# Optimization experiments

Hardware: AMD Instinct MI355X
Metric: run time of the kernel (lower is better)

The kernel has to match this reference:

```python
import jax, jax.numpy as jnp
import numpy as np

DIM = 2048
H = 16
KVH = 4
HD = DIM // H          # 128
G = H // KVH           # 4
EPS = 1e-6


def _rmsnorm(x, w):
    rms = jnp.sqrt(jnp.mean(x * x, axis=-1, keepdims=True) + EPS)
    return x / rms * w


def setup_inputs() -> dict:
    key = jax.random.key(0)
    ks = jax.random.split(key, 9)
    B, S = 4, 2048
    query = jax.random.normal(ks[0], (B, S, DIM), dtype=jnp.float32)
    key_t = jax.random.normal(ks[1], (B, S, DIM), dtype=jnp.float32)
    value = jax.random.normal(ks[2], (B, S, DIM), dtype=jnp.float32)
    sc = 1.0 / np.sqrt(DIM)
    Wq = jax.random.normal(ks[3], (DIM, DIM), dtype=jnp.float32) * sc
    Wk = jax.random.normal(ks[4], (KVH * HD, DIM), dtype=jnp.float32) * sc
    Wv = jax.random.normal(ks[5], (KVH * HD, DIM), dtype=jnp.float32) * sc
    Wo = jax.random.normal(ks[6], (DIM, DIM), dtype=jnp.float32) * sc
    norm_q_w = jnp.ones((HD,), dtype=jnp.float32)
    norm_k_w = jnp.ones((HD,), dtype=jnp.float32)
    return {"query": query, "key": key_t, "value": value,
            "Wq": Wq, "Wk": Wk, "Wv": Wv, "Wo": Wo,
            "norm_q_w": norm_q_w, "norm_k_w": norm_k_w}


def reference(query, key, value, Wq, Wk, Wv, Wo, norm_q_w, norm_k_w):
    B, S, _ = query.shape
    Skv = key.shape[1]
    scale = HD ** -0.5
    # projections (torch Linear: x @ W.T)
    q = (query @ Wq.T).reshape(B, S, H, HD)
    k = (key @ Wk.T).reshape(B, Skv, KVH, HD)
    v = (value @ Wv.T).reshape(B, Skv, KVH, HD)
    # fused QK RMSNorm over head_dim
    q = _rmsnorm(q, norm_q_w)
    k = _rmsnorm(k, norm_k_w)
    # GQA: group query heads as (KVH, G); repeat_interleave maps q head
    # h = kv*G + g to kv head kv, which this reshape reproduces exactly.
    q = q.transpose(0, 2, 1, 3).reshape(B, KVH, G, S, HD)
    k = k.transpose(0, 2, 1, 3)  # [B, KVH, Skv, HD]
    v = v.transpose(0, 2, 1, 3)
    scores = jnp.einsum('bkgsd,bktd->bkgst', q, k) * scale
    attn = jax.nn.softmax(scores, axis=-1)
    out = jnp.einsum('bkgst,bktd->bkgsd', attn, v)
    # back to [B, S, H*HD] with head order (kv, g)
    out = out.transpose(0, 3, 1, 2, 4).reshape(B, S, DIM)
    return out @ Wo.T
```

## Files before the change

### kernel.cpp

```cpp
#include <hip/hip_runtime.h>
#include <hip/hip_bf16.h>


typedef short short8 __attribute__((ext_vector_type(8)));
typedef short8 short8a __attribute__((may_alias));
typedef short short4v __attribute__((ext_vector_type(4)));
typedef short4v short4a __attribute__((may_alias));
typedef float f32x4 __attribute__((ext_vector_type(4)));
typedef float float4v __attribute__((ext_vector_type(4)));
typedef unsigned int uinta __attribute__((may_alias));
typedef unsigned short u16;

__device__ __forceinline__ u16 f2bf(float x) {
    unsigned u = __float_as_uint(x);
    u += 0x7fffu + ((u >> 16) & 1u);
    return (u16)(u >> 16);
}
__device__ __forceinline__ float bf2f(u16 b) {
    return __uint_as_float(((unsigned)b) << 16);
}
__device__ __forceinline__ void lds_load16(void* lds, const void* g) {
    __builtin_amdgcn_global_load_lds(
        (__attribute__((address_space(1))) unsigned int*)g,
        (__attribute__((address_space(3))) unsigned int*)lds, 16, 0, 0);
}

__global__ void detect_dtype(const unsigned* __restrict__ q, int* __restrict__ flag)
{
    unsigned bits = q[threadIdx.x];
    unsigned e = (bits >> 23) & 0xffu;
    bool sane = (e >= 90u && e <= 160u);
    unsigned long long m = __ballot(sane);
    if (threadIdx.x == 0) *flag = (__popcll(m) >= 48) ? 1 : 0;
}

#define BN 128
#define BK 32

template<int RT>
__global__ __launch_bounds__(256)
void gemm_bt(const void* __restrict__ Ap, const void* __restrict__ Bp,
             void* __restrict__ Cp, const int* __restrict__ flagp,
             int M, int N, int K, int a_mode, int b_mode, int o_mode)
{
    constexpr int BM = RT * 32;
    __shared__ __attribute__((aligned(16))) u16 As[BM * BK];
    __shared__ __attribute__((aligned(16))) u16 Bs[BN * BK];
    const int f     = *flagp;
    const bool af32 = a_mode && f;
    const bool bf32 = b_mode && f;
    const bool of32 = o_mode && f;
    const int tid  = threadIdx.x;
    const int wave = tid >> 6;
    const int lane = tid & 63;
    const int lrow = lane & 15;
    const int quad = lane >> 4;
    const int wm   = (wave >> 1) * (RT * 16);
    const int wn   = (wave & 1) * 64;
    const int m0   = blockIdx.y * BM;
    const int n0   = blockIdx.x * BN;
    const int sel  = (lrow >> 1) & 3;

    f32x4 acc[RT][4] = {};

    for (int k0 = 0; k0 < K; k0 += BK) {
        __syncthreads();
        if (!af32) {
            for (int p = 0; p < RT / 2; ++p) {
                int seg = wave * (RT / 2) + p;
                int row = seg * 16 + (lane >> 2);
                int gch = (lane & 3) ^ ((row >> 1) & 3);
                lds_load16(&As[seg * 16 * BK],
                           (const u16*)Ap + (size_t)(m0 + row) * K + k0 + gch * 8);
            }
        } else {
            for (int it = 0; it < RT / 2; ++it) {
                int idx = tid + it * 256;
                int row = idx >> 2;
                int c   = idx & 3;
                int gch = c ^ ((row >> 1) & 3);
                const float* gp = (const float*)Ap + (size_t)(m0 + row) * K + k0 + gch * 8;
                float4v x0 = *(const float4v*)gp;
                float4v x1 = *(const float4v*)(gp + 4);
                short8 v;
                for (int i = 0; i < 4; ++i) { v[i] = (short)f2bf(x0[i]); v[i + 4] = (short)f2bf(x1[i]); }
                *(short8a*)(&As[row * BK + c * 8]) = v;
            }
        }
        if (!bf32) {
            for (int p = 0; p < 2; ++p) {
                int seg = wave * 2 + p;
                int row = seg * 16 + (lane >> 2);
                int gch = (lane & 3) ^ ((row >> 1) & 3);
                lds_load16(&Bs[seg * 16 * BK],
                           (const u16*)Bp + (size_t)(n0 + row) * K + k0 + gch * 8);
            }
        } else {
            for (int it = 0; it < 2; ++it) {
                int idx = tid + it * 256;
                int row = idx >> 2;
                int c   = idx & 3;
                int gch = c ^ ((row >> 1) & 3);
                const float* gp = (const float*)Bp + (size_t)(n0 + row) * K + k0 + gch * 8;
                float4v x0 = *(const float4v*)gp;
                float4v x1 = *(const float4v*)(gp + 4);
                short8 v;
                for (int i = 0; i < 4; ++i) { v[i] = (short)f2bf(x0[i]); v[i + 4] = (short)f2bf(x1[i]); }
                *(short8a*)(&Bs[row * BK + c * 8]) = v;
            }
        }
        __builtin_amdgcn_s_waitcnt(0);
        __syncthreads();

        short8 afr[RT], bfr[4];
        for (int i = 0; i < RT; ++i)
            afr[i] = *(const short8a*)(&As[(wm + i * 16 + lrow) * BK + (quad ^ sel) * 8]);
        for (int j = 0; j < 4; ++j)
            bfr[j] = *(const short8a*)(&Bs[(wn + j * 16 + lrow) * BK + (quad ^ sel) * 8]);
        for (int i = 0; i < RT; ++i)
            for (int j = 0; j < 4; ++j)
                acc[i][j] = __builtin_amdgcn_mfma_f32_16x16x32_bf16(afr[i], bfr[j], acc[i][j], 0, 0, 0);
    }

    for (int i = 0; i < RT; ++i)
        for (int j = 0; j < 4; ++j)
            for (int r = 0; r < 4; ++r) {
                int row = m0 + wm + i * 16 + quad * 4 + r;
                int col = n0 + wn + j * 16 + lrow;
                size_t idx = (size_t)row * N + col;
                float v = acc[i][j][r];
                if (of32) ((float*)Cp)[idx] = v;
                else      ((u16*)Cp)[idx]   = f2bf(v);
            }
}

__global__ __launch_bounds__(256)
void rmsnorm128v(u16* __restrict__ X, const void* __restrict__ w,
                 const int* __restrict__ flagp, float outscale)
{
    const int f = *flagp;
    int t     = blockIdx.x * 256 + threadIdx.x;
    int chunk = t >> 4;
    int l16   = t & 15;
    u16* xp = X + (size_t)chunk * 128 + l16 * 8;
    short8 xv = *(const short8a*)xp;
    float xs[8]; float ss = 0.f;
    for (int i = 0; i < 8; ++i) { xs[i] = bf2f((u16)xv[i]); ss += xs[i] * xs[i]; }
    ss += __shfl_xor(ss, 1); ss += __shfl_xor(ss, 2);
    ss += __shfl_xor(ss, 4); ss += __shfl_xor(ss, 8);
    float inv = outscale * rsqrtf(ss * (1.0f / 128.0f) + 1e-6f);
    float ws[8];
    if (f) {
        float4v w0 = ((const float4v*)w)[l16 * 2];
        float4v w1 = ((const float4v*)w)[l16 * 2 + 1];
        for (int i = 0; i < 4; ++i) { ws[i] = w0[i]; ws[i + 4] = w1[i]; }
    } else {
        short8 wv = ((const short8a*)w)[l16];
        for (int i = 0; i < 8; ++i) ws[i] = bf2f((u16)wv[i]);
    }
    short8 o;
    for (int i = 0; i < 8; ++i) o[i] = (short)f2bf(xs[i] * inv * ws[i]);
    *(short8a*)xp = o;
}

#define VTS 72

__global__ __launch_bounds__(256, 4)
void attn_fused(const u16* __restrict__ Q, const u16* __restrict__ Kb,
                const u16* __restrict__ Vb, u16* __restrict__ O,
                int Sq, int Skv)
{
    __shared__ __attribute__((aligned(16))) u16 Ks[64 * 128];
    __shared__ __attribute__((aligned(16))) u16 Vt[128 * VTS];
    const int qt   = blockIdx.x;
    const int kvh  = blockIdx.y;
    const int b    = blockIdx.z;
    const int tid  = threadIdx.x;
    const int wave = tid >> 6;
    const int lane = tid & 63;
    const int lrow = lane & 15;
    const int quad = lane >> 4;
    const int h    = kvh * 4 + wave;
    const int q0   = qt * 16;
    const int swz  = lrow & 7;

    short8 qf[4];
    {
        const u16* qp = Q + (size_t)(b * Sq + q0 + lrow) * 2048 + h * 128 + quad * 8;
        for (int ks = 0; ks < 4; ++ks) qf[ks] = *(const short8a*)(qp + ks * 32);
    }

    float lsum = 0.f;
    f32x4 oacc[8] = {};

    for (int t0 = 0; t0 < Skv; t0 += 64) {
        __syncthreads();
        for (int p = 0; p < 4; ++p) {
            int seg = p * 4 + wave;
            int row = seg * 4 + (lane >> 4);
            int gch = (lane & 15) ^ (row & 7);
            lds_load16(&Ks[seg * 4 * 128],
                       Kb + (size_t)(b * Skv + t0 + row) * 512 + kvh * 128 + gch * 8);
        }
        for (int rr = 0; rr < 2; ++rr) {
            int idx = tid + rr * 256;
            int p   = idx & 31;
            int d0  = (idx >> 5) * 8;
            const u16* vp = Vb + (size_t)(b * Skv + t0 + 2 * p) * 512 + kvh * 128 + d0;
            short8 v0 = *(const short8a*)vp;
            short8 v1 = *(const short8a*)(vp + 512);
            for (int i = 0; i < 8; ++i) {
                unsigned pr = (unsigned)(u16)v0[i] | ((unsigned)(u16)v1[i] << 16);
                *(uinta*)(&Vt[(d0 + i) * VTS + 2 * p]) = pr;
            }
        }
        __builtin_amdgcn_s_waitcnt(0);
        __syncthreads();

        for (int nt = 0; nt < 4; ++nt) {
            f32x4 sacc = {};
            for (int ks = 0; ks < 4; ++ks) {
                short8 kf = *(const short8a*)(
                    &Ks[(nt * 16 + lrow) * 128 + ((ks * 4 + quad) ^ swz) * 8]);
                sacc = __builtin_amdgcn_mfma_f32_16x16x32_bf16(kf, qf[ks], sacc, 0, 0, 0);
            }
            float p0 = exp2f(sacc[0]), p1 = exp2f(sacc[1]);
            float p2 = exp2f(sacc[2]), p3 = exp2f(sacc[3]);
            lsum += (p0 + p1) + (p2 + p3);
            short4v pf;
            pf[0] = (short)f2bf(p0); pf[1] = (short)f2bf(p1);
            pf[2] = (short)f2bf(p2); pf[3] = (short)f2bf(p3);
            for (int dblk = 0; dblk < 8; ++dblk) {
                short4v av = *(const short4a*)(
                    &Vt[(dblk * 16 + lrow) * VTS + nt * 16 + quad * 4]);
                oacc[dblk] = __builtin_amdgcn_mfma_f32_16x16x16bf16_1k(av, pf, oacc[dblk], 0, 0, 0);
            }
        }
    }

    lsum += __shfl_xor(lsum, 16);
    lsum += __shfl_xor(lsum, 32);
    float inv = 1.0f / lsum;

    {
        u16* op = O + (size_t)(b * Sq + q0 + lrow) * 2048 + h * 128 + quad * 4;
        for (int dblk = 0; dblk < 8; ++dblk) {
            unsigned w0 = (unsigned)f2bf(oacc[dblk][0] * inv) |
                          ((unsigned)f2bf(oacc[dblk][1] * inv) << 16);
            unsigned w1 = (unsigned)f2bf(oacc[dblk][2] * inv) |
                          ((unsigned)f2bf(oacc[dblk][3] * inv) << 16);
            uint2 wv; wv.x = w0; wv.y = w1;
            *(uint2*)(op + dblk * 16) = wv;
        }
    }
}

extern "C" void kernel_launch(void* const* d_in, const int* in_sizes, int n_in,
                              void* d_out, int out_size, void* d_ws, size_t ws_size,
                              hipStream_t stream)
{
    const int M  = in_sizes[0] / 2048;
    const int Sq = 2048;
    const int Bb = M / Sq;

    char* ws = (char*)d_ws;
    int* flag = (int*)ws;
    u16* Qb = (u16*)(ws + 256);
    u16* Kb = (u16*)(ws + 256 + (size_t)M * 2048 * 2);
    u16* Vb = (u16*)(ws + 256 + (size_t)M * 2048 * 2 + (size_t)M * 512 * 2);
    u16* Ob = (u16*)(ws + 256 + (size_t)M * 2048 * 2 + (size_t)M * 512 * 4);

    dim3 blk(256);
    detect_dtype<<<1, 64, 0, stream>>>((const unsigned*)d_in[0], flag);
    gemm_bt<4><<<dim3(2048 / BN, M / 128), blk, 0, stream>>>(d_in[0], d_in[3], Qb, flag, M, 2048, 2048, 1, 1, 0);
    gemm_bt<2><<<dim3(512 / BN,  M / 64),  blk, 0, stream>>>(d_in[1], d_in[4], Kb, flag, M, 512, 2048, 1, 1, 0);
    gemm_bt<2><<<dim3(512 / BN,  M / 64),  blk, 0, stream>>>(d_in[2], d_in[5], Vb, flag, M, 512, 2048, 1, 1, 0);
    rmsnorm128v<<<dim3(M),     blk, 0, stream>>>(Qb, d_in[7], flag, 0.12752227653159732f);
    rmsnorm128v<<<dim3(M / 4), blk, 0, stream>>>(Kb, d_in[8], flag, 1.0f);
    attn_fused<<<dim3(Sq / 16, 4, Bb), blk, 0, stream>>>(Qb, Kb, Vb, Ob, Sq, Sq);
    gemm_bt<4><<<dim3(2048 / BN, M / 128), blk, 0, stream>>>(Ob, d_in[6], d_out, flag, M, 2048, 2048, 0, 1, 1);
}
```

Before: 991.5 us.

## Switch attention to 32x32x16 MFMA with pre-transposed V from projection GEMM

```diff
diff --git a/kernel.cpp b/kernel.cpp
--- a/kernel.cpp
+++ b/kernel.cpp
@@ -4,9 +4,8 @@
 
 typedef short short8 __attribute__((ext_vector_type(8)));
 typedef short8 short8a __attribute__((may_alias));
-typedef short short4v __attribute__((ext_vector_type(4)));
-typedef short4v short4a __attribute__((may_alias));
 typedef float f32x4 __attribute__((ext_vector_type(4)));
+typedef float f32x16 __attribute__((ext_vector_type(16)));
 typedef float float4v __attribute__((ext_vector_type(4)));
 typedef unsigned int uinta __attribute__((may_alias));
 typedef unsigned short u16;
@@ -18,6 +17,12 @@
 }
 __device__ __forceinline__ float bf2f(u16 b) {
     return __uint_as_float(((unsigned)b) << 16);
+}
+__device__ __forceinline__ unsigned pk2bf(float lo, float hi) {
+    float2 t; t.x = lo; t.y = hi;
+    __hip_bfloat162 h = __float22bfloat162_rn(t);
+    union { __hip_bfloat162 h; unsigned u; } c; c.h = h;
+    return c.u;
 }
 __device__ __forceinline__ void lds_load16(void* lds, const void* g) {
     __builtin_amdgcn_global_load_lds(
@@ -49,7 +54,7 @@
     const int f     = *flagp;
     const bool af32 = a_mode && f;
     const bool bf32 = b_mode && f;
-    const bool of32 = o_mode && f;
+    const bool of32 = (o_mode == 1) && f;
     const int tid  = threadIdx.x;
     const int wave = tid >> 6;
     const int lane = tid & 63;
@@ -127,10 +132,16 @@
             for (int r = 0; r < 4; ++r) {
                 int row = m0 + wm + i * 16 + quad * 4 + r;
                 int col = n0 + wn + j * 16 + lrow;
-                size_t idx = (size_t)row * N + col;
                 float v = acc[i][j][r];
-                if (of32) ((float*)Cp)[idx] = v;
-                else      ((u16*)Cp)[idx]   = f2bf(v);
+                if (o_mode == 2) {
+                    size_t fidx = ((size_t)(((row >> 11) * 4 + (col >> 7)) * 128
+                                   + (col & 127))) * 2048 + (row & 2047);
+                    ((u16*)Cp)[fidx] = f2bf(v);
+                } else {
+                    size_t idx = (size_t)row * N + col;
+                    if (of32) ((float*)Cp)[idx] = v;
+                    else      ((u16*)Cp)[idx]   = f2bf(v);
+                }
             }
 }
 
@@ -163,95 +174,104 @@
     *(short8a*)xp = o;
 }
 
-#define VTS 72
-
-__global__ __launch_bounds__(256, 4)
+
+__global__ __launch_bounds__(256)
 void attn_fused(const u16* __restrict__ Q, const u16* __restrict__ Kb,
-                const u16* __restrict__ Vb, u16* __restrict__ O,
+                const u16* __restrict__ Vt, u16* __restrict__ O,
                 int Sq, int Skv)
 {
     __shared__ __attribute__((aligned(16))) u16 Ks[64 * 128];
-    __shared__ __attribute__((aligned(16))) u16 Vt[128 * VTS];
+    __shared__ __attribute__((aligned(16))) u16 Vs[128 * 64];
     const int qt   = blockIdx.x;
     const int kvh  = blockIdx.y;
     const int b    = blockIdx.z;
     const int tid  = threadIdx.x;
     const int wave = tid >> 6;
     const int lane = tid & 63;
-    const int lrow = lane & 15;
-    const int quad = lane >> 4;
+    const int q    = lane & 31;
+    const int L    = lane >> 5;
     const int h    = kvh * 4 + wave;
-    const int q0   = qt * 16;
-    const int swz  = lrow & 7;
-
-    short8 qf[4];
+    const int q0   = qt * 32;
+
+    short8 qf[8];
     {
-        const u16* qp = Q + (size_t)(b * Sq + q0 + lrow) * 2048 + h * 128 + quad * 8;
-        for (int ks = 0; ks < 4; ++ks) qf[ks] = *(const short8a*)(qp + ks * 32);
+        const u16* qp = Q + (size_t)(b * Sq + q0 + q) * 2048 + h * 128 + L * 8;
+        for (int kd = 0; kd < 8; ++kd) qf[kd] = *(const short8a*)(qp + kd * 16);
     }
 
     float lsum = 0.f;
-    f32x4 oacc[8] = {};
+    f32x16 oacc[4] = {};
+
+    const int krow  = wave * 16 + (lane >> 4);
+    const int kch   = lane & 15;
+    const int vrow  = wave * 32 + (lane >> 3);
+    const int vch   = lane & 7;
+    const u16* kbase = Kb + (size_t)b * Skv * 512 + kvh * 128;
+    const u16* vbase = Vt + (size_t)((b * 4 + kvh) * 128) * 2048;
 
     for (int t0 = 0; t0 < Skv; t0 += 64) {
         __syncthreads();
         for (int p = 0; p < 4; ++p) {
-            int seg = p * 4 + wave;
-            int row = seg * 4 + (lane >> 4);
-            int gch = (lane & 15) ^ (row & 7);
-            lds_load16(&Ks[seg * 4 * 128],
-                       Kb + (size_t)(b * Skv + t0 + row) * 512 + kvh * 128 + gch * 8);
-        }
-        for (int rr = 0; rr < 2; ++rr) {
-            int idx = tid + rr * 256;
-            int p   = idx & 31;
-            int d0  = (idx >> 5) * 8;
-            const u16* vp = Vb + (size_t)(b * Skv + t0 + 2 * p) * 512 + kvh * 128 + d0;
-            short8 v0 = *(const short8a*)vp;
-            short8 v1 = *(const short8a*)(vp + 512);
-            for (int i = 0; i < 8; ++i) {
-                unsigned pr = (unsigned)(u16)v0[i] | ((unsigned)(u16)v1[i] << 16);
-                *(uinta*)(&Vt[(d0 + i) * VTS + 2 * p]) = pr;
-            }
+            int lr  = krow + p * 4 - ((lane >> 4) ? 0 : 0);
+            int ldsrow = wave * 16 + p * 4 + (lane >> 4);
+            (void)lr;
+            int tl  = (ldsrow & 32) + (((ldsrow >> 4) & 1) << 4)
+                    + (((ldsrow >> 2) & 1) << 3) + (((ldsrow >> 3) & 1) << 2)
+                    + (ldsrow & 3);
+            int gch = kch ^ (ldsrow & 7);
+            lds_load16(&Ks[(wave * 16 + p * 4) * 128],
+                       kbase + (size_t)(t0 + tl) * 512 + gch * 8);
+        }
+        for (int p = 0; p < 4; ++p) {
+            int drow = wave * 32 + p * 8 + (lane >> 3);
+            int gch  = vch ^ (drow & 7);
+            lds_load16(&Vs[(wave * 32 + p * 8) * 64],
+                       vbase + (size_t)drow * 2048 + t0 + gch * 8);
         }
         __builtin_amdgcn_s_waitcnt(0);
         __syncthreads();
 
-        for (int nt = 0; nt < 4; ++nt) {
-            f32x4 sacc = {};
-            for (int ks = 0; ks < 4; ++ks) {
+        for (int n32 = 0; n32 < 2; ++n32) {
+            f32x16 sacc = {};
+            for (int kd = 0; kd < 8; ++kd) {
                 short8 kf = *(const short8a*)(
-                    &Ks[(nt * 16 + lrow) * 128 + ((ks * 4 + quad) ^ swz) * 8]);
-                sacc = __builtin_amdgcn_mfma_f32_16x16x32_bf16(kf, qf[ks], sacc, 0, 0, 0);
-            }
-            float p0 = exp2f(sacc[0]), p1 = exp2f(sacc[1]);
-            float p2 = exp2f(sacc[2]), p3 = exp2f(sacc[3]);
-            lsum += (p0 + p1) + (p2 + p3);
-            short4v pf;
-            pf[0] = (short)f2bf(p0); pf[1] = (short)f2bf(p1);
-            pf[2] = (short)f2bf(p2); pf[3] = (short)f2bf(p3);
-            for (int dblk = 0; dblk < 8; ++dblk) {
-                short4v av = *(const short4a*)(
-                    &Vt[(dblk * 16 + lrow) * VTS + nt * 16 + quad * 4]);
-                oacc[dblk] = __builtin_amdgcn_mfma_f32_16x16x16bf16_1k(av, pf, oacc[dblk], 0, 0, 0);
-            }
-        }
-    }
-
-    lsum += __shfl_xor(lsum, 16);
+                    &Ks[(n32 * 32 + q) * 128 + (((kd * 2 + L) ^ (lane & 7)) * 8)]);
+                sacc = __builtin_amdgcn_mfma_f32_32x32x16_bf16(kf, qf[kd], sacc, 0, 0, 0);
+            }
+            for (int kb2 = 0; kb2 < 2; ++kb2) {
+                float p0 = exp2f(sacc[kb2 * 8 + 0]), p1 = exp2f(sacc[kb2 * 8 + 1]);
+                float p2 = exp2f(sacc[kb2 * 8 + 2]), p3 = exp2f(sacc[kb2 * 8 + 3]);
+                float p4 = exp2f(sacc[kb2 * 8 + 4]), p5 = exp2f(sacc[kb2 * 8 + 5]);
+                float p6 = exp2f(sacc[kb2 * 8 + 6]), p7 = exp2f(sacc[kb2 * 8 + 7]);
+                lsum += ((p0 + p1) + (p2 + p3)) + ((p4 + p5) + (p6 + p7));
+                union { short8 s; unsigned u[4]; } pf;
+                pf.u[0] = pk2bf(p0, p1); pf.u[1] = pk2bf(p2, p3);
+                pf.u[2] = pk2bf(p4, p5); pf.u[3] = pk2bf(p6, p7);
+                for (int dblk = 0; dblk < 4; ++dblk) {
+                    short8 vf = *(const short8a*)(
+                        &Vs[(dblk * 32 + q) * 64
+                            + (((n32 * 4 + kb2 * 2 + L) ^ (lane & 7)) * 8)]);
+                    oacc[dblk] = __builtin_amdgcn_mfma_f32_32x32x16_bf16(
+                        vf, pf.s, oacc[dblk], 0, 0, 0);
+                }
+            }
+        }
+    }
+
     lsum += __shfl_xor(lsum, 32);
     float inv = 1.0f / lsum;
 
     {
-        u16* op = O + (size_t)(b * Sq + q0 + lrow) * 2048 + h * 128 + quad * 4;
-        for (int dblk = 0; dblk < 8; ++dblk) {
-            unsigned w0 = (unsigned)f2bf(oacc[dblk][0] * inv) |
-                          ((unsigned)f2bf(oacc[dblk][1] * inv) << 16);
-            unsigned w1 = (unsigned)f2bf(oacc[dblk][2] * inv) |
-                          ((unsigned)f2bf(oacc[dblk][3] * inv) << 16);
-            uint2 wv; wv.x = w0; wv.y = w1;
-            *(uint2*)(op + dblk * 16) = wv;
-        }
+        u16* op = O + (size_t)(b * Sq + q0 + q) * 2048 + h * 128 + L * 4;
+        for (int dblk = 0; dblk < 4; ++dblk)
+            for (int rg = 0; rg < 4; ++rg) {
+                unsigned w0 = pk2bf(oacc[dblk][rg * 4 + 0] * inv,
+                                    oacc[dblk][rg * 4 + 1] * inv);
+                unsigned w1 = pk2bf(oacc[dblk][rg * 4 + 2] * inv,
+                                    oacc[dblk][rg * 4 + 3] * inv);
+                uint2 wv; wv.x = w0; wv.y = w1;
+                *(uint2*)(op + dblk * 32 + rg * 8) = wv;
+            }
     }
 }
 
@@ -274,9 +294,9 @@
     detect_dtype<<<1, 64, 0, stream>>>((const unsigned*)d_in[0], flag);
     gemm_bt<4><<<dim3(2048 / BN, M / 128), blk, 0, stream>>>(d_in[0], d_in[3], Qb, flag, M, 2048, 2048, 1, 1, 0);
     gemm_bt<2><<<dim3(512 / BN,  M / 64),  blk, 0, stream>>>(d_in[1], d_in[4], Kb, flag, M, 512, 2048, 1, 1, 0);
-    gemm_bt<2><<<dim3(512 / BN,  M / 64),  blk, 0, stream>>>(d_in[2], d_in[5], Vb, flag, M, 512, 2048, 1, 1, 0);
+    gemm_bt<2><<<dim3(512 / BN,  M / 64),  blk, 0, stream>>>(d_in[2], d_in[5], Vb, flag, M, 512, 2048, 1, 1, 2);
     rmsnorm128v<<<dim3(M),     blk, 0, stream>>>(Qb, d_in[7], flag, 0.12752227653159732f);
     rmsnorm128v<<<dim3(M / 4), blk, 0, stream>>>(Kb, d_in[8], flag, 1.0f);
-    attn_fused<<<dim3(Sq / 16, 4, Bb), blk, 0, stream>>>(Qb, Kb, Vb, Ob, Sq, Sq);
+    attn_fused<<<dim3(Sq / 32, 4, Bb), blk, 0, stream>>>(Qb, Kb, Vb, Ob, Sq, Sq);
     gemm_bt<4><<<dim3(2048 / BN, M / 128), blk, 0, stream>>>(Ob, d_in[6], d_out, flag, M, 2048, 2048, 0, 1, 1);
 }
```

Measured after the change: 3.085 ms. 3.11x slower.
